# Kernel optimization log

Measured on AMD Instinct MI355X. Metric: run time of the kernel, lower is better.

## Reference

```python
import jax, jax.numpy as jnp
import numpy as np

H = 128      # hidden_dim
D = 2        # data_dim
T = 20       # obs_len
B = 16384    # batch
PRED = 30    # pred_len
LN_EPS = 1e-5


def _lstm_cell(x, h, c, Wih, Whh, bih, bhh):
    # torch gate order: i, f, g, o
    gates = x @ Wih.T + h @ Whh.T + bih + bhh
    i, f, g, o = jnp.split(gates, 4, axis=-1)
    c = jax.nn.sigmoid(f) * c + jax.nn.sigmoid(i) * jnp.tanh(g)
    h = jax.nn.sigmoid(o) * jnp.tanh(c)
    return h, c


def _encode(seq, Wih, Whh, bih, bhh):
    # seq: [T, B, D]; return final (h, c)
    b = seq.shape[1]
    h0 = jnp.zeros((b, H), seq.dtype)
    def step(carry, x):
        h, c = _lstm_cell(x, carry[0], carry[1], Wih, Whh, bih, bhh)
        return (h, c), None
    (h, c), _ = jax.lax.scan(step, (h0, h0), seq)
    return h, c


def _layernorm(x, g, b):
    m = jnp.mean(x, axis=-1, keepdims=True)
    v = jnp.var(x, axis=-1, keepdims=True)
    return (x - m) * jax.lax.rsqrt(v + LN_EPS) * g + b


def setup_inputs() -> dict:
    key = jax.random.key(0)
    ks = jax.random.split(key, 20)
    s_in = 1.0 / np.sqrt(H)  # torch default LSTM init scale
    def W(k, shape):
        return jax.random.normal(k, shape, jnp.float32) * s_in
    return {
        "pos": jax.random.normal(ks[0], (T, B, D), jnp.float32),
        "speed": jax.random.normal(ks[1], (T, B, D), jnp.float32),
        "Wih_pe": W(ks[2], (4 * H, D)), "Whh_pe": W(ks[3], (4 * H, H)),
        "bih_pe": W(ks[4], (4 * H,)), "bhh_pe": W(ks[5], (4 * H,)),
        "Wih_se": W(ks[6], (4 * H, D)), "Whh_se": W(ks[7], (4 * H, H)),
        "bih_se": W(ks[8], (4 * H,)), "bhh_se": W(ks[9], (4 * H,)),
        "ln_g": jnp.ones((H,), jnp.float32), "ln_b": jnp.zeros((H,), jnp.float32),
        "Wih_sd": W(ks[10], (4 * H, D)), "Whh_sd": W(ks[11], (4 * H, H)),
        "bih_sd": W(ks[12], (4 * H,)), "bhh_sd": W(ks[13], (4 * H,)),
        "Wih_pd": W(ks[14], (4 * H, D)), "Whh_pd": W(ks[15], (4 * H, H)),
        "bih_pd": W(ks[16], (4 * H,)), "bhh_pd": W(ks[17], (4 * H,)),
        "Wfc": W(ks[18], (D, H)), "bfc": jnp.zeros((D,), jnp.float32),
    }


def reference(pos, speed, Wih_pe, Whh_pe, bih_pe, bhh_pe,
              Wih_se, Whh_se, bih_se, bhh_se, ln_g, ln_b,
              Wih_sd, Whh_sd, bih_sd, bhh_sd,
              Wih_pd, Whh_pd, bih_pd, bhh_pd, Wfc, bfc):
    hpo, cpo = _encode(pos, Wih_pe, Whh_pe, bih_pe, bhh_pe)
    hpo = _layernorm(hpo, ln_g, ln_b)
    cpo = _layernorm(cpo, ln_g, ln_b)
    hsp, csp = _encode(speed, Wih_se, Whh_se, bih_se, bhh_se)
    hsp = _layernorm(hsp, ln_g, ln_b)
    csp = _layernorm(csp, ln_g, ln_b)

    # concat_features=False path
    hds, cds = hpo + hsp, cpo + csp
    curr_speed, curr_pos = speed[-1], pos[-1]

    def step(carry, _):
        hds, cds, hpo, cpo, cs, cp = carry
        hds, cds = _lstm_cell(cs, hds, cds, Wih_sd, Whh_sd, bih_sd, bhh_sd)
        cs = hds @ Wfc.T + bfc
        hpo, cpo = _lstm_cell(cp, hpo, cpo, Wih_pd, Whh_pd, bih_pd, bhh_pd)
        cp = hpo @ Wfc.T + bfc
        return (hds, cds, hpo, cpo, cs, cp), (cp, cs)

    _, (pos_out, speed_out) = jax.lax.scan(
        step, (hds, cds, hpo, cpo, curr_speed, curr_pos), None, length=PRED)
    return pos_out, speed_out  # each [PRED, B, D]
```

## Files before the change

### kernel.cpp

```cpp
#include <hip/hip_runtime.h>

#define H 128
#define D 2
#define T_OBS 20
#define BATCH 16384
#define PRED 30
#define M 32
#define NTH 512
#define HP 136
#define FP 132
#define LN_EPS 1e-5f
#define LOG2E  1.442695041f
#define LOG2E2 2.885390082f

typedef __attribute__((ext_vector_type(8))) _Float16 half8_t;
typedef __attribute__((ext_vector_type(2))) _Float16 half2_t;
typedef __attribute__((ext_vector_type(4))) float float4_t;

__device__ __forceinline__ float fast_rcp(float x){ return __builtin_amdgcn_rcpf(x); }
__device__ __forceinline__ float exp2_f(float x){ return __builtin_amdgcn_exp2f(x); }

__device__ __forceinline__ void lds_barrier(){
  asm volatile("s_waitcnt lgkmcnt(0)\n\ts_barrier" ::: "memory");
}

struct PhaseConsts {
  half8_t bw[4][4];
  float bs[4], w0[4], w1[4];
};

__device__ __forceinline__ void load_phase(PhaseConsts& P, const float* __restrict__ Whh,
                                           const float* __restrict__ Wih,
                                           const float* __restrict__ bih,
                                           const float* __restrict__ bhh,
                                           int wv, int l15, int q){
#pragma unroll
  for(int g=0; g<4; g++){
    const float sc = (g==2) ? LOG2E2 : LOG2E;
    const int n = g*H + 16*wv + l15;
    P.bs[g] = (bih[n] + bhh[n]) * sc;
    P.w0[g] = Wih[n*D + 0] * sc;
    P.w1[g] = Wih[n*D + 1] * sc;
#pragma unroll
    for(int ks=0; ks<4; ks++){
      const float* p = Whh + (size_t)n*H + ks*32 + q*8;
      float4 a = *(const float4*)p;
      float4 b = *(const float4*)(p+4);
      half8_t f;
      f[0]=(_Float16)(a.x*sc); f[1]=(_Float16)(a.y*sc); f[2]=(_Float16)(a.z*sc); f[3]=(_Float16)(a.w*sc);
      f[4]=(_Float16)(b.x*sc); f[5]=(_Float16)(b.y*sc); f[6]=(_Float16)(b.z*sc); f[7]=(_Float16)(b.w*sc);
      P.bw[g][ks] = f;
    }
  }
}

__device__ __forceinline__ void load_phase_dec(PhaseConsts& P, const float* __restrict__ Whh,
                                               const float* __restrict__ Wih,
                                               const float* __restrict__ bih,
                                               const float* __restrict__ bhh,
                                               const float* __restrict__ Wfc,
                                               const float* __restrict__ bfc,
                                               int wv, int l15, int q){
#pragma unroll
  for(int g=0; g<4; g++){
    const float sc = (g==2) ? LOG2E2 : LOG2E;
    const int n = g*H + 16*wv + l15;
    const float wi0 = Wih[n*D + 0];
    const float wi1 = Wih[n*D + 1];
    P.bs[g] = fmaf(wi1, bfc[1], fmaf(wi0, bfc[0], bih[n] + bhh[n])) * sc;
    P.w0[g] = wi0 * sc;
    P.w1[g] = wi1 * sc;
#pragma unroll
    for(int ks=0; ks<4; ks++){
      const float* p  = Whh + (size_t)n*H + ks*32 + q*8;
      const float* f0 = Wfc + 0*H + ks*32 + q*8;
      const float* f1 = Wfc + 1*H + ks*32 + q*8;
      half8_t f;
#pragma unroll
      for(int j=0;j<8;j++){
        f[j] = (_Float16)(fmaf(wi1, f1[j], fmaf(wi0, f0[j], p[j])) * sc);
      }
      P.bw[g][ks] = f;
    }
  }
}

template<bool HASX>
__device__ __forceinline__ void cell_step(_Float16 (*hsh)[M][HP], int cur,
                                          const float* __restrict__ xsrc,
                                          const PhaseConsts& P, float (&c)[2][4],
                                          int wv, int l15, int q){
  float4_t acc[2][4];
  if constexpr (HASX){
#pragma unroll
    for(int mh=0; mh<2; mh++){
      float x0[4], x1[4];
#pragma unroll
      for(int r=0; r<4; r++){
        x0[r] = xsrc[(mh*16 + 4*q+r)*2 + 0];
        x1[r] = xsrc[(mh*16 + 4*q+r)*2 + 1];
      }
#pragma unroll
      for(int g=0; g<4; g++)
#pragma unroll
        for(int r=0; r<4; r++)
          acc[mh][g][r] = fmaf(P.w1[g], x1[r], fmaf(P.w0[g], x0[r], P.bs[g]));
    }
  } else {
#pragma unroll
    for(int mh=0; mh<2; mh++)
#pragma unroll
      for(int g=0; g<4; g++)
#pragma unroll
        for(int r=0; r<4; r++)
          acc[mh][g][r] = P.bs[g];
  }

#pragma unroll
  for(int ks=0; ks<4; ks++){
#pragma unroll
    for(int mh=0; mh<2; mh++){
      const half8_t a = *(const half8_t*)&hsh[cur][mh*16 + l15][ks*32 + q*8];
#pragma unroll
      for(int g=0; g<4; g++){
        acc[mh][g] = __builtin_amdgcn_mfma_f32_16x16x32_f16(a, P.bw[g][ks], acc[mh][g], 0,0,0);
      }
    }
  }
  const int nxt = cur ^ 1;
  const int u = 16*wv + l15;
#pragma unroll
  for(int mh=0; mh<2; mh++){
#pragma unroll
    for(int r=0; r<4; r++){
      const float Ei = exp2_f(-acc[mh][0][r]);
      const float Ef = exp2_f(-acc[mh][1][r]);
      const float Eg = exp2_f( acc[mh][2][r]);
      const float Eo = exp2_f(-acc[mh][3][r]);
      const float tf  = 1.f + Ef;
      const float dig = (Eg + 1.f) * (1.f + Ei);
      const float m1  = (Eg - 1.f) * tf;
      const float num = fmaf(c[mh][r], dig, m1);
      const float den = dig * tf;
      const float cc  = num * fast_rcp(den);
      c[mh][r] = cc;
      const float ccl = fminf(cc, 30.f);
      const float Ecc = exp2_f(ccl * LOG2E2);
      const float d2  = (Ecc + 1.f) * (1.f + Eo);
      const float hv  = (Ecc - 1.f) * fast_rcp(d2);
      const int m = mh*16 + 4*q + r;
      hsh[nxt][m][u] = (_Float16)hv;
    }
  }
  lds_barrier();
}

__device__ __forceinline__ void layernorm32(const float (*src)[FP], float (*dst)[FP],
                                            const float* __restrict__ g,
                                            const float* __restrict__ b, int tid){
  const int m = tid >> 4, sub = tid & 15;
  float v[8];
  float s = 0.f, s2 = 0.f;
#pragma unroll
  for(int j=0;j<8;j++){ v[j] = src[m][sub*8+j]; s += v[j]; s2 = fmaf(v[j], v[j], s2); }
#pragma unroll
  for(int msk=1; msk<16; msk<<=1){ s += __shfl_xor(s, msk, 64); s2 += __shfl_xor(s2, msk, 64); }
  const float mean = s * (1.f/H);
  const float var  = fmaf(-mean, mean, s2 * (1.f/H));
  const float inv  = rsqrtf(var + LN_EPS);
#pragma unroll
  for(int j=0;j<8;j++){
    const int u = sub*8+j;
    dst[m][u] = fmaf((v[j]-mean)*inv, g[u], b[u]);
  }
}

__device__ __forceinline__ void fc_out(const _Float16 (*hb)[HP], const _Float16 (*wfch)[H],
                                       const float* __restrict__ bfcs,
                                       float* __restrict__ gout, int row0, int tid){
  const int m = tid >> 4, d = (tid >> 3) & 1, ch = tid & 7;
  const half2_t* hp2 = (const half2_t*)&hb[m][ch*16];
  const half2_t* wp2 = (const half2_t*)&wfch[d][ch*16];
  float s = 0.f;
#pragma unroll
  for(int j=0;j<8;j++) s = __builtin_amdgcn_fdot2(hp2[j], wp2[j], s, false);
  s += __shfl_xor(s, 1, 64); s += __shfl_xor(s, 2, 64); s += __shfl_xor(s, 4, 64);
  if(ch == 0){
    gout[(size_t)(row0+m)*D + d] = s + bfcs[d];
  }
}

__device__ __forceinline__ void fc_delta(const _Float16 (*hb)[HP], const float (*wfc)[H],
                                         const float* __restrict__ bfcs,
                                         const float* __restrict__ xlast,
                                         float (*xb)[D], int tid){
  const int m = tid >> 4, d = (tid >> 3) & 1, ch = tid & 7;
  const _Float16* hp = &hb[m][ch*16];
  float s = 0.f;
#pragma unroll
  for(int j=0;j<16;j++) s = fmaf((float)hp[j], wfc[d][ch*16+j], s);
  s += __shfl_xor(s, 1, 64); s += __shfl_xor(s, 2, 64); s += __shfl_xor(s, 4, 64);
  if(ch == 0){
    xb[m][d] = xlast[m*D + d] - (s + bfcs[d]);
  }
}

__global__ __launch_bounds__(NTH, 2) void traj_kernel(
    const float* __restrict__ pos, const float* __restrict__ speed,
    const float* __restrict__ Wih_pe, const float* __restrict__ Whh_pe,
    const float* __restrict__ bih_pe, const float* __restrict__ bhh_pe,
    const float* __restrict__ Wih_se, const float* __restrict__ Whh_se,
    const float* __restrict__ bih_se, const float* __restrict__ bhh_se,
    const float* __restrict__ ln_g, const float* __restrict__ ln_b,
    const float* __restrict__ Wih_sd, const float* __restrict__ Whh_sd,
    const float* __restrict__ bih_sd, const float* __restrict__ bhh_sd,
    const float* __restrict__ Wih_pd, const float* __restrict__ Whh_pd,
    const float* __restrict__ bih_pd, const float* __restrict__ bhh_pd,
    const float* __restrict__ Wfc, const float* __restrict__ bfc,
    float* __restrict__ out)
{
  __shared__ __align__(16) _Float16 hsh[2][M][HP];
  __shared__ float tmpf[M][FP];
  __shared__ float hpoN[M][FP];
  __shared__ float cpoN[M][FP];
  __shared__ float seqx[2][T_OBS][M][D];
  __shared__ float xbuf[M][D];
  __shared__ float wfcs[D][H];
  __shared__ __align__(16) _Float16 wfch[D][H];
  __shared__ float bfcs[2];

  const int tid  = threadIdx.x;
  const int lane = tid & 63;
  const int wv   = tid >> 6;
  const int q    = lane >> 4;
  const int l15  = lane & 15;
  const int row0 = blockIdx.x * M;
  const int u    = 16*wv + l15;

  for(int idx = tid; idx < 2*T_OBS*M*D; idx += NTH){
    const int chain = idx / (T_OBS*M*D);
    const int rem   = idx % (T_OBS*M*D);
    const int t = rem / (M*D), e = rem % (M*D);
    const float* src = chain ? speed : pos;
    seqx[chain][t][e>>1][e&1] = src[(size_t)t*BATCH*D + row0*D + e];
  }
  if(tid < D*H){
    wfcs[tid>>7][tid&127] = Wfc[tid];
    wfch[tid>>7][tid&127] = (_Float16)Wfc[tid];
  }
  if(tid < 2)   bfcs[tid] = bfc[tid];
  { int* hz = (int*)&hsh[0][0][0];
    for(int idx = tid; idx < M*HP/2; idx += NTH) hz[idx] = 0; }

  PhaseConsts P;
  float c[2][4];
  load_phase(P, Whh_pe, Wih_pe, bih_pe, bhh_pe, wv, l15, q);
#pragma unroll
  for(int mh=0;mh<2;mh++)
#pragma unroll
    for(int r=0;r<4;r++) c[mh][r] = 0.f;
  __syncthreads();

  int cur = 0;
  for(int t=0; t<T_OBS; t++){ cell_step<true>(hsh, cur, &seqx[0][t][0][0], P, c, wv, l15, q); cur ^= 1; }
  for(int idx=tid; idx<M*H; idx+=NTH){
    const int m = idx>>7, uu = idx&127;
    tmpf[m][uu] = (float)hsh[cur][m][uu];
  }
  __syncthreads();
  layernorm32(tmpf, hpoN, ln_g, ln_b, tid);
  __syncthreads();
#pragma unroll
  for(int mh=0;mh<2;mh++)
#pragma unroll
    for(int r=0;r<4;r++) tmpf[mh*16 + 4*q+r][u] = c[mh][r];
  __syncthreads();
  layernorm32(tmpf, cpoN, ln_g, ln_b, tid);
  __syncthreads();

  load_phase(P, Whh_se, Wih_se, bih_se, bhh_se, wv, l15, q);
#pragma unroll
  for(int mh=0;mh<2;mh++)
#pragma unroll
    for(int r=0;r<4;r++) c[mh][r] = 0.f;
  for(int idx=tid; idx<M*H; idx+=NTH){
    const int m = idx>>7, uu = idx&127;
    hsh[0][m][uu] = (_Float16)0.f;
  }
  cur = 0;
  __syncthreads();
  for(int t=0; t<T_OBS; t++){ cell_step<true>(hsh, cur, &seqx[1][t][0][0], P, c, wv, l15, q); cur ^= 1; }
  for(int idx=tid; idx<M*H; idx+=NTH){
    const int m = idx>>7, uu = idx&127;
    tmpf[m][uu] = (float)hsh[cur][m][uu];
  }
  __syncthreads();
  layernorm32(tmpf, tmpf, ln_g, ln_b, tid);
  __syncthreads();
  for(int idx=tid; idx<M*H; idx+=NTH){
    const int m = idx>>7, uu = idx&127;
    hsh[0][m][uu] = (_Float16)(tmpf[m][uu] + hpoN[m][uu]);
  }
  __syncthreads();
#pragma unroll
  for(int mh=0;mh<2;mh++)
#pragma unroll
    for(int r=0;r<4;r++) tmpf[mh*16 + 4*q+r][u] = c[mh][r];
  __syncthreads();
  layernorm32(tmpf, tmpf, ln_g, ln_b, tid);
  __syncthreads();
#pragma unroll
  for(int mh=0;mh<2;mh++)
#pragma unroll
    for(int r=0;r<4;r++) c[mh][r] = tmpf[mh*16 + 4*q+r][u] + cpoN[mh*16 + 4*q+r][u];

  load_phase_dec(P, Whh_sd, Wih_sd, bih_sd, bhh_sd, Wfc, bfc, wv, l15, q);
  fc_delta(hsh[0], wfcs, bfcs, &seqx[1][T_OBS-1][0][0], xbuf, tid);
  __syncthreads();

  float* spd_out = out + (size_t)PRED*BATCH*D;
  cur = 0;
  cell_step<true>(hsh, cur, &xbuf[0][0], P, c, wv, l15, q);
  fc_out(hsh[cur^1], wfch, bfcs, spd_out, row0, tid);
  cur ^= 1;
  for(int t=1; t<PRED; t++){
    cell_step<false>(hsh, cur, nullptr, P, c, wv, l15, q);
    fc_out(hsh[cur^1], wfch, bfcs, spd_out + (size_t)t*BATCH*D, row0, tid);
    cur ^= 1;
  }
  __syncthreads();

  for(int idx=tid; idx<M*H; idx+=NTH){
    const int m = idx>>7, uu = idx&127;
    hsh[0][m][uu] = (_Float16)hpoN[m][uu];
  }
#pragma unroll
  for(int mh=0;mh<2;mh++)
#pragma unroll
    for(int r=0;r<4;r++) c[mh][r] = cpoN[mh*16 + 4*q+r][u];
  load_phase_dec(P, Whh_pd, Wih_pd, bih_pd, bhh_pd, Wfc, bfc, wv, l15, q);
  __syncthreads();
  fc_delta(hsh[0], wfcs, bfcs, &seqx[0][T_OBS-1][0][0], xbuf, tid);
  __syncthreads();

  cur = 0;
  cell_step<true>(hsh, cur, &xbuf[0][0], P, c, wv, l15, q);
  fc_out(hsh[cur^1], wfch, bfcs, out, row0, tid);
  cur ^= 1;
  for(int t=1; t<PRED; t++){
    cell_step<false>(hsh, cur, nullptr, P, c, wv, l15, q);
    fc_out(hsh[cur^1], wfch, bfcs, out + (size_t)t*BATCH*D, row0, tid);
    cur ^= 1;
  }
}

extern "C" void kernel_launch(void* const* d_in, const int* in_sizes, int n_in,
                              void* d_out, int out_size, void* d_ws, size_t ws_size,
                              hipStream_t stream)
{
  const float* pos    = (const float*)d_in[0];
  const float* speed  = (const float*)d_in[1];
  const float* Wih_pe = (const float*)d_in[2];
  const float* Whh_pe = (const float*)d_in[3];
  const float* bih_pe = (const float*)d_in[4];
  const float* bhh_pe = (const float*)d_in[5];
  const float* Wih_se = (const float*)d_in[6];
  const float* Whh_se = (const float*)d_in[7];
  const float* bih_se = (const float*)d_in[8];
  const float* bhh_se = (const float*)d_in[9];
  const float* ln_g   = (const float*)d_in[10];
  const float* ln_b   = (const float*)d_in[11];
  const float* Wih_sd = (const float*)d_in[12];
  const float* Whh_sd = (const float*)d_in[13];
  const float* bih_sd = (const float*)d_in[14];
  const float* bhh_sd = (const float*)d_in[15];
  const float* Wih_pd = (const float*)d_in[16];
  const float* Whh_pd = (const float*)d_in[17];
  const float* bih_pd = (const float*)d_in[18];
  const float* bhh_pd = (const float*)d_in[19];
  const float* Wfc    = (const float*)d_in[20];
  const float* bfc    = (const float*)d_in[21];

  traj_kernel<<<BATCH/M, NTH, 0, stream>>>(
      pos, speed, Wih_pe, Whh_pe, bih_pe, bhh_pe,
      Wih_se, Whh_se, bih_se, bhh_se, ln_g, ln_b,
      Wih_sd, Whh_sd, bih_sd, bhh_sd, Wih_pd, Whh_pd, bih_pd, bhh_pd,
      Wfc, bfc, (float*)d_out);
}
```

Baseline: 497.4 us.

## Split LSTM gates across two wave groups with LDS exchange of gate pre-activations

```diff
diff --git a/kernel.cpp b/kernel.cpp
--- a/kernel.cpp
+++ b/kernel.cpp
@@ -6,7 +6,7 @@
 #define BATCH 16384
 #define PRED 30
 #define M 32
-#define NTH 512
+#define NTH 1024
 #define HP 136
 #define FP 132
 #define LN_EPS 1e-5f
@@ -24,23 +24,24 @@
   asm volatile("s_waitcnt lgkmcnt(0)\n\ts_barrier" ::: "memory");
 }
 
-struct PhaseConsts {
-  half8_t bw[4][4];
-  float bs[4], w0[4], w1[4];
+struct PhaseConsts2 {
+  half8_t bw[2][4];
+  float bs[2], w0[2], w1[2];
 };
 
-__device__ __forceinline__ void load_phase(PhaseConsts& P, const float* __restrict__ Whh,
-                                           const float* __restrict__ Wih,
-                                           const float* __restrict__ bih,
-                                           const float* __restrict__ bhh,
-                                           int wv, int l15, int q){
-#pragma unroll
-  for(int g=0; g<4; g++){
-    const float sc = (g==2) ? LOG2E2 : LOG2E;
-    const int n = g*H + 16*wv + l15;
-    P.bs[g] = (bih[n] + bhh[n]) * sc;
-    P.w0[g] = Wih[n*D + 0] * sc;
-    P.w1[g] = Wih[n*D + 1] * sc;
+__device__ __forceinline__ void load_phase2(PhaseConsts2& P, const float* __restrict__ Whh,
+                                            const float* __restrict__ Wih,
+                                            const float* __restrict__ bih,
+                                            const float* __restrict__ bhh,
+                                            int ug, int gp, int l15, int q){
+#pragma unroll
+  for(int gi=0; gi<2; gi++){
+    const int ga = 2*gp + gi;
+    const float sc = (ga==2) ? LOG2E2 : LOG2E;
+    const int n = ga*H + 16*ug + l15;
+    P.bs[gi] = (bih[n] + bhh[n]) * sc;
+    P.w0[gi] = Wih[n*D + 0] * sc;
+    P.w1[gi] = Wih[n*D + 1] * sc;
 #pragma unroll
     for(int ks=0; ks<4; ks++){
       const float* p = Whh + (size_t)n*H + ks*32 + q*8;
@@ -49,27 +50,28 @@
       half8_t f;
       f[0]=(_Float16)(a.x*sc); f[1]=(_Float16)(a.y*sc); f[2]=(_Float16)(a.z*sc); f[3]=(_Float16)(a.w*sc);
       f[4]=(_Float16)(b.x*sc); f[5]=(_Float16)(b.y*sc); f[6]=(_Float16)(b.z*sc); f[7]=(_Float16)(b.w*sc);
-      P.bw[g][ks] = f;
+      P.bw[gi][ks] = f;
     }
   }
 }
 
-__device__ __forceinline__ void load_phase_dec(PhaseConsts& P, const float* __restrict__ Whh,
-                                               const float* __restrict__ Wih,
-                                               const float* __restrict__ bih,
-                                               const float* __restrict__ bhh,
-                                               const float* __restrict__ Wfc,
-                                               const float* __restrict__ bfc,
-                                               int wv, int l15, int q){
-#pragma unroll
-  for(int g=0; g<4; g++){
-    const float sc = (g==2) ? LOG2E2 : LOG2E;
-    const int n = g*H + 16*wv + l15;
+__device__ __forceinline__ void load_phase2_dec(PhaseConsts2& P, const float* __restrict__ Whh,
+                                                const float* __restrict__ Wih,
+                                                const float* __restrict__ bih,
+                                                const float* __restrict__ bhh,
+                                                const float* __restrict__ Wfc,
+                                                const float* __restrict__ bfc,
+                                                int ug, int gp, int l15, int q){
+#pragma unroll
+  for(int gi=0; gi<2; gi++){
+    const int ga = 2*gp + gi;
+    const float sc = (ga==2) ? LOG2E2 : LOG2E;
+    const int n = ga*H + 16*ug + l15;
     const float wi0 = Wih[n*D + 0];
     const float wi1 = Wih[n*D + 1];
-    P.bs[g] = fmaf(wi1, bfc[1], fmaf(wi0, bfc[0], bih[n] + bhh[n])) * sc;
-    P.w0[g] = wi0 * sc;
-    P.w1[g] = wi1 * sc;
+    P.bs[gi] = fmaf(wi1, bfc[1], fmaf(wi0, bfc[0], bih[n] + bhh[n])) * sc;
+    P.w0[gi] = wi0 * sc;
+    P.w1[gi] = wi1 * sc;
 #pragma unroll
     for(int ks=0; ks<4; ks++){
       const float* p  = Whh + (size_t)n*H + ks*32 + q*8;
@@ -80,7 +82,7 @@
       for(int j=0;j<8;j++){
         f[j] = (_Float16)(fmaf(wi1, f1[j], fmaf(wi0, f0[j], p[j])) * sc);
       }
-      P.bw[g][ks] = f;
+      P.bw[gi][ks] = f;
     }
   }
 }
@@ -88,9 +90,10 @@
 template<bool HASX>
 __device__ __forceinline__ void cell_step(_Float16 (*hsh)[M][HP], int cur,
                                           const float* __restrict__ xsrc,
-                                          const PhaseConsts& P, float (&c)[2][4],
-                                          int wv, int l15, int q){
-  float4_t acc[2][4];
+                                          const PhaseConsts2& P, float (&c)[4],
+                                          float (*xch)[8][64],
+                                          int wv, int gp, int l15, int q, int lane, int u){
+  float4_t acc[2][2];
   if constexpr (HASX){
 #pragma unroll
     for(int mh=0; mh<2; mh++){
@@ -101,19 +104,19 @@
         x1[r] = xsrc[(mh*16 + 4*q+r)*2 + 1];
       }
 #pragma unroll
-      for(int g=0; g<4; g++)
+      for(int gi=0; gi<2; gi++)
 #pragma unroll
         for(int r=0; r<4; r++)
-          acc[mh][g][r] = fmaf(P.w1[g], x1[r], fmaf(P.w0[g], x0[r], P.bs[g]));
+          acc[mh][gi][r] = fmaf(P.w1[gi], x1[r], fmaf(P.w0[gi], x0[r], P.bs[gi]));
     }
   } else {
 #pragma unroll
     for(int mh=0; mh<2; mh++)
 #pragma unroll
-      for(int g=0; g<4; g++)
+      for(int gi=0; gi<2; gi++)
 #pragma unroll
         for(int r=0; r<4; r++)
-          acc[mh][g][r] = P.bs[g];
+          acc[mh][gi][r] = P.bs[gi];
   }
 
 #pragma unroll
@@ -122,35 +125,47 @@
     for(int mh=0; mh<2; mh++){
       const half8_t a = *(const half8_t*)&hsh[cur][mh*16 + l15][ks*32 + q*8];
 #pragma unroll
-      for(int g=0; g<4; g++){
-        acc[mh][g] = __builtin_amdgcn_mfma_f32_16x16x32_f16(a, P.bw[g][ks], acc[mh][g], 0,0,0);
+      for(int gi=0; gi<2; gi++){
+        acc[mh][gi] = __builtin_amdgcn_mfma_f32_16x16x32_f16(a, P.bw[gi][ks], acc[mh][gi], 0,0,0);
       }
     }
   }
+
+  const int omh = 1 - gp;
+#pragma unroll
+  for(int gi=0; gi<2; gi++)
+#pragma unroll
+    for(int r=0; r<4; r++)
+      xch[wv][gi*4 + r][lane] = acc[omh][gi][r];
+  lds_barrier();
+
+  float pg0[4], pg1[4];
+#pragma unroll
+  for(int r=0; r<4; r++){ pg0[r] = xch[wv^8][r][lane]; pg1[r] = xch[wv^8][4+r][lane]; }
+
   const int nxt = cur ^ 1;
-  const int u = 16*wv + l15;
-#pragma unroll
-  for(int mh=0; mh<2; mh++){
-#pragma unroll
-    for(int r=0; r<4; r++){
-      const float Ei = exp2_f(-acc[mh][0][r]);
-      const float Ef = exp2_f(-acc[mh][1][r]);
-      const float Eg = exp2_f( acc[mh][2][r]);
-      const float Eo = exp2_f(-acc[mh][3][r]);
-      const float tf  = 1.f + Ef;
-      const float dig = (Eg + 1.f) * (1.f + Ei);
-      const float m1  = (Eg - 1.f) * tf;
-      const float num = fmaf(c[mh][r], dig, m1);
-      const float den = dig * tf;
-      const float cc  = num * fast_rcp(den);
-      c[mh][r] = cc;
-      const float ccl = fminf(cc, 30.f);
-      const float Ecc = exp2_f(ccl * LOG2E2);
-      const float d2  = (Ecc + 1.f) * (1.f + Eo);
-      const float hv  = (Ecc - 1.f) * fast_rcp(d2);
-      const int m = mh*16 + 4*q + r;
-      hsh[nxt][m][u] = (_Float16)hv;
-    }
+  const int mrow = gp*16 + 4*q;
+#pragma unroll
+  for(int r=0; r<4; r++){
+    float ai, af, ag, ao;
+    if(gp == 0){ ai = acc[0][0][r]; af = acc[0][1][r]; ag = pg0[r];        ao = pg1[r]; }
+    else       { ai = pg0[r];       af = pg1[r];       ag = acc[1][0][r];  ao = acc[1][1][r]; }
+    const float Ei = exp2_f(-ai);
+    const float Ef = exp2_f(-af);
+    const float Eg = exp2_f( ag);
+    const float Eo = exp2_f(-ao);
+    const float tf  = 1.f + Ef;
+    const float dig = (Eg + 1.f) * (1.f + Ei);
+    const float m1  = (Eg - 1.f) * tf;
+    const float num = fmaf(c[r], dig, m1);
+    const float den = dig * tf;
+    const float cc  = num * fast_rcp(den);
+    c[r] = cc;
+    const float ccl = fminf(cc, 30.f);
+    const float Ecc = exp2_f(ccl * LOG2E2);
+    const float d2  = (Ecc + 1.f) * (1.f + Eo);
+    const float hv  = (Ecc - 1.f) * fast_rcp(d2);
+    hsh[nxt][mrow + r][u] = (_Float16)hv;
   }
   lds_barrier();
 }
@@ -158,6 +173,7 @@
 __device__ __forceinline__ void layernorm32(const float (*src)[FP], float (*dst)[FP],
                                             const float* __restrict__ g,
                                             const float* __restrict__ b, int tid){
+  if(tid >= 512) return;
   const int m = tid >> 4, sub = tid & 15;
   float v[8];
   float s = 0.f, s2 = 0.f;
@@ -178,6 +194,7 @@
 __device__ __forceinline__ void fc_out(const _Float16 (*hb)[HP], const _Float16 (*wfch)[H],
                                        const float* __restrict__ bfcs,
                                        float* __restrict__ gout, int row0, int tid){
+  if(tid >= 512) return;
   const int m = tid >> 4, d = (tid >> 3) & 1, ch = tid & 7;
   const half2_t* hp2 = (const half2_t*)&hb[m][ch*16];
   const half2_t* wp2 = (const half2_t*)&wfch[d][ch*16];
@@ -194,6 +211,7 @@
                                          const float* __restrict__ bfcs,
                                          const float* __restrict__ xlast,
                                          float (*xb)[D], int tid){
+  if(tid >= 512) return;
   const int m = tid >> 4, d = (tid >> 3) & 1, ch = tid & 7;
   const _Float16* hp = &hb[m][ch*16];
   float s = 0.f;
@@ -205,7 +223,7 @@
   }
 }
 
-__global__ __launch_bounds__(NTH, 2) void traj_kernel(
+__global__ __launch_bounds__(NTH, 1) void traj_kernel(
     const float* __restrict__ pos, const float* __restrict__ speed,
     const float* __restrict__ Wih_pe, const float* __restrict__ Whh_pe,
     const float* __restrict__ bih_pe, const float* __restrict__ bhh_pe,
@@ -228,14 +246,17 @@
   __shared__ float wfcs[D][H];
   __shared__ __align__(16) _Float16 wfch[D][H];
   __shared__ float bfcs[2];
+  __shared__ float xch[16][8][64];
 
   const int tid  = threadIdx.x;
   const int lane = tid & 63;
   const int wv   = tid >> 6;
+  const int ug   = wv & 7;
+  const int gp   = wv >> 3;
   const int q    = lane >> 4;
   const int l15  = lane & 15;
   const int row0 = blockIdx.x * M;
-  const int u    = 16*wv + l15;
+  const int u    = 16*ug + l15;
 
   for(int idx = tid; idx < 2*T_OBS*M*D; idx += NTH){
     const int chain = idx / (T_OBS*M*D);
@@ -252,17 +273,15 @@
   { int* hz = (int*)&hsh[0][0][0];
     for(int idx = tid; idx < M*HP/2; idx += NTH) hz[idx] = 0; }
 
-  PhaseConsts P;
-  float c[2][4];
-  load_phase(P, Whh_pe, Wih_pe, bih_pe, bhh_pe, wv, l15, q);
-#pragma unroll
-  for(int mh=0;mh<2;mh++)
-#pragma unroll
-    for(int r=0;r<4;r++) c[mh][r] = 0.f;
+  PhaseConsts2 P;
+  float c[4];
+  load_phase2(P, Whh_pe, Wih_pe, bih_pe, bhh_pe, ug, gp, l15, q);
+#pragma unroll
+  for(int r=0;r<4;r++) c[r] = 0.f;
   __syncthreads();
 
   int cur = 0;
-  for(int t=0; t<T_OBS; t++){ cell_step<true>(hsh, cur, &seqx[0][t][0][0], P, c, wv, l15, q); cur ^= 1; }
+  for(int t=0; t<T_OBS; t++){ cell_step<true>(hsh, cur, &seqx[0][t][0][0], P, c, xch, wv, gp, l15, q, lane, u); cur ^= 1; }
   for(int idx=tid; idx<M*H; idx+=NTH){
     const int m = idx>>7, uu = idx&127;
     tmpf[m][uu] = (float)hsh[cur][m][uu];
@@ -271,25 +290,21 @@
   layernorm32(tmpf, hpoN, ln_g, ln_b, tid);
   __syncthreads();
 #pragma unroll
-  for(int mh=0;mh<2;mh++)
-#pragma unroll
-    for(int r=0;r<4;r++) tmpf[mh*16 + 4*q+r][u] = c[mh][r];
+  for(int r=0;r<4;r++) tmpf[gp*16 + 4*q+r][u] = c[r];
   __syncthreads();
   layernorm32(tmpf, cpoN, ln_g, ln_b, tid);
   __syncthreads();
 
-  load_phase(P, Whh_se, Wih_se, bih_se, bhh_se, wv, l15, q);
-#pragma unroll
-  for(int mh=0;mh<2;mh++)
-#pragma unroll
-    for(int r=0;r<4;r++) c[mh][r] = 0.f;
+  load_phase2(P, Whh_se, Wih_se, bih_se, bhh_se, ug, gp, l15, q);
+#pragma unroll
+  for(int r=0;r<4;r++) c[r] = 0.f;
   for(int idx=tid; idx<M*H; idx+=NTH){
     const int m = idx>>7, uu = idx&127;
     hsh[0][m][uu] = (_Float16)0.f;
   }
   cur = 0;
   __syncthreads();
-  for(int t=0; t<T_OBS; t++){ cell_step<true>(hsh, cur, &seqx[1][t][0][0], P, c, wv, l15, q); cur ^= 1; }
+  for(int t=0; t<T_OBS; t++){ cell_step<true>(hsh, cur, &seqx[1][t][0][0], P, c, xch, wv, gp, l15, q, lane, u); cur ^= 1; }
   for(int idx=tid; idx<M*H; idx+=NTH){
     const int m = idx>>7, uu = idx&127;
     tmpf[m][uu] = (float)hsh[cur][m][uu];
@@ -303,28 +318,24 @@
   }
   __syncthreads();
 #pragma unroll
-  for(int mh=0;mh<2;mh++)
-#pragma unroll
-    for(int r=0;r<4;r++) tmpf[mh*16 + 4*q+r][u] = c[mh][r];
+  for(int r=0;r<4;r++) tmpf[gp*16 + 4*q+r][u] = c[r];
   __syncthreads();
   layernorm32(tmpf, tmpf, ln_g, ln_b, tid);
   __syncthreads();
 #pragma unroll
-  for(int mh=0;mh<2;mh++)
-#pragma unroll
-    for(int r=0;r<4;r++) c[mh][r] = tmpf[mh*16 + 4*q+r][u] + cpoN[mh*16 + 4*q+r][u];
-
-  load_phase_dec(P, Whh_sd, Wih_sd, bih_sd, bhh_sd, Wfc, bfc, wv, l15, q);
+  for(int r=0;r<4;r++) c[r] = tmpf[gp*16 + 4*q+r][u] + cpoN[gp*16 + 4*q+r][u];
+
+  load_phase2_dec(P, Whh_sd, Wih_sd, bih_sd, bhh_sd, Wfc, bfc, ug, gp, l15, q);
   fc_delta(hsh[0], wfcs, bfcs, &seqx[1][T_OBS-1][0][0], xbuf, tid);
   __syncthreads();
 
   float* spd_out = out + (size_t)PRED*BATCH*D;
   cur = 0;
-  cell_step<true>(hsh, cur, &xbuf[0][0], P, c, wv, l15, q);
+  cell_step<true>(hsh, cur, &xbuf[0][0], P, c, xch, wv, gp, l15, q, lane, u);
   fc_out(hsh[cur^1], wfch, bfcs, spd_out, row0, tid);
   cur ^= 1;
   for(int t=1; t<PRED; t++){
-    cell_step<false>(hsh, cur, nullptr, P, c, wv, l15, q);
+    cell_step<false>(hsh, cur, nullptr, P, c, xch, wv, gp, l15, q, lane, u);
     fc_out(hsh[cur^1], wfch, bfcs, spd_out + (size_t)t*BATCH*D, row0, tid);
     cur ^= 1;
   }
@@ -335,20 +346,18 @@
     hsh[0][m][uu] = (_Float16)hpoN[m][uu];
   }
 #pragma unroll
-  for(int mh=0;mh<2;mh++)
-#pragma unroll
-    for(int r=0;r<4;r++) c[mh][r] = cpoN[mh*16 + 4*q+r][u];
-  load_phase_dec(P, Whh_pd, Wih_pd, bih_pd, bhh_pd, Wfc, bfc, wv, l15, q);
+  for(int r=0;r<4;r++) c[r] = cpoN[gp*16 + 4*q+r][u];
+  load_phase2_dec(P, Whh_pd, Wih_pd, bih_pd, bhh_pd, Wfc, bfc, ug, gp, l15, q);
   __syncthreads();
   fc_delta(hsh[0], wfcs, bfcs, &seqx[0][T_OBS-1][0][0], xbuf, tid);
   __syncthreads();
 
   cur = 0;
-  cell_step<true>(hsh, cur, &xbuf[0][0], P, c, wv, l15, q);
+  cell_step<true>(hsh, cur, &xbuf[0][0], P, c, xch, wv, gp, l15, q, lane, u);
   fc_out(hsh[cur^1], wfch, bfcs, out, row0, tid);
   cur ^= 1;
   for(int t=1; t<PRED; t++){
-    cell_step<false>(hsh, cur, nullptr, P, c, wv, l15, q);
+    cell_step<false>(hsh, cur, nullptr, P, c, xch, wv, gp, l15, q, lane, u);
     fc_out(hsh[cur^1], wfch, bfcs, out + (size_t)t*BATCH*D, row0, tid);
     cur ^= 1;
   }
```

Result: slower. 961.9 us (+93.4%).
